# Performance work log

Hardware: AMD Instinct MI355X
Metric: run time of the kernel (lower is better)

## Reference

```python
import jax, jax.numpy as jnp
import numpy as np

B, E, P, L, D = 16, 2048, 16384, 5, 64  # batch, num_edges, num node-pairs, max_path_distance, edge_dim
EPS = 1e-9


def setup_inputs() -> dict:
    key = jax.random.key(0)
    k1, k2, k3 = jax.random.split(key, 3)
    edge_embedding = jax.random.normal(k1, (B, E, D), dtype=jnp.float32)
    # -1 marks padding (unused path slots), valid entries in [0, E)
    edge_paths = jax.random.randint(k2, (B, P, L), -1, E, dtype=jnp.int64)
    edge_vector = jax.random.normal(k3, (L, D), dtype=jnp.float32)
    return {"edge_embedding": edge_embedding, "edge_paths": edge_paths, "edge_vector": edge_vector}


def reference(edge_embedding, edge_paths, edge_vector):
    # edge_embedding: (B, E, D); edge_paths: (B, P, L) int with -1 padding; edge_vector: (L, D)
    edge_mask = edge_paths == -1                                     # (B, P, L)
    clamped = jnp.clip(edge_paths, 0, None)
    # batched gather: out[b, p, l, :] = edge_embedding[b, clamped[b, p, l], :]
    gathered = jax.vmap(lambda emb, idx: emb[idx])(edge_embedding, clamped)  # (B, P, L, D)
    gathered = jnp.where(edge_mask[..., None], jnp.zeros((), gathered.dtype), gathered)
    path_lengths = (~edge_mask).sum(axis=-1).astype(edge_embedding.dtype) + EPS  # (B, P)
    enc = jnp.einsum('beld,ld->be', gathered, edge_vector)           # (B, P)
    return enc / path_lengths
```

## Files before the change

### kernel.cpp

```cpp
#include <hip/hip_runtime.h>
#include <hip/hip_bf16.h>

#define B 16
#define E 2048
#define P 16384
#define L 5
#define D 64
#define EPS 1e-9f

__global__ __launch_bounds__(256) void edge_proj_kernel(
    const float* __restrict__ emb, const float* __restrict__ ev,
    float* __restrict__ proj) {
    __shared__ float sev[L * D];
    for (int i = threadIdx.x; i < L * D; i += 256) sev[i] = ev[i];
    __syncthreads();

    int gid  = blockIdx.x * 256 + threadIdx.x;
    int row  = gid >> 1;
    int half = gid & 1;

    const float4* src = (const float4*)(emb + (size_t)row * D + half * 32);
    const float4* w4  = (const float4*)sev;

    float acc[L] = {0.f, 0.f, 0.f, 0.f, 0.f};
#pragma unroll
    for (int c = 0; c < 8; ++c) {
        float4 v = src[c];
#pragma unroll
        for (int l = 0; l < L; ++l) {
            float4 w = w4[l * 16 + half * 8 + c];
            acc[l] += v.x * w.x + v.y * w.y + v.z * w.z + v.w * w.w;
        }
    }
#pragma unroll
    for (int l = 0; l < L; ++l) acc[l] += __shfl_xor(acc[l], 1);

    if (half == 0) {
        float* p = proj + (size_t)row * L;
#pragma unroll
        for (int l = 0; l < L; ++l) p[l] = acc[l];
    }
}

__global__ __launch_bounds__(256) void edge_gather_kernel(
    const int* __restrict__ paths, const float* __restrict__ proj,
    float* __restrict__ out) {
    __shared__ float sproj[E * L];
    int b = blockIdx.x & 15;
    int g = blockIdx.x >> 4;

    const float4* src = (const float4*)(proj + (size_t)b * E * L);
    float4* dst = (float4*)sproj;
#pragma unroll
    for (int i = 0; i < (E * L) / 4 / 256; ++i)
        dst[threadIdx.x + i * 256] = src[threadIdx.x + i * 256];
    __syncthreads();

    int pbase = g * (P / 16);
#pragma unroll
    for (int k = 0; k < 4; ++k) {
        int p = pbase + k * 256 + threadIdx.x;
        const int* pp = paths + ((size_t)b * P + p) * L;
        float sum = 0.f;
        int cnt = 0;
#pragma unroll
        for (int l = 0; l < L; ++l) {
            int e = pp[l];
            bool valid = (e >= 0);
            int ec = valid ? e : 0;
            float v = sproj[ec * L + l];
            sum += valid ? v : 0.f;
            cnt += valid ? 1 : 0;
        }
        out[(size_t)b * P + p] = sum / ((float)cnt + EPS);
    }
}

extern "C" void kernel_launch(void* const* d_in, const int* in_sizes, int n_in,
                              void* d_out, int out_size, void* d_ws, size_t ws_size,
                              hipStream_t stream) {
    const float* emb   = (const float*)d_in[0];
    const int*   paths = (const int*)d_in[1];
    const float* ev    = (const float*)d_in[2];
    float* out  = (float*)d_out;
    float* proj = (float*)d_ws;

    edge_proj_kernel<<<(2 * B * E) / 256, 256, 0, stream>>>(emb, ev, proj);
    edge_gather_kernel<<<16 * B, 256, 0, stream>>>(paths, proj, out);
}
```

Baseline: 68.47 us.

## Fuse edge projection into gather kernel with per-block recomputation

Merges the projection and gather kernels into one launch: each block recomputes the per-edge projections for its batch directly into shared memory, then performs the path gather. This removes a kernel launch and the global workspace round-trip for the projection. In exchange, each of the 16 blocks per batch redundantly reads the full batch embedding and redoes the projection, with many accumulators per thread and strided row reads.

```diff
diff --git a/kernel.cpp b/kernel.cpp
--- a/kernel.cpp
+++ b/kernel.cpp
@@ -8,59 +8,62 @@
 #define D 64
 #define EPS 1e-9f
 
-__global__ __launch_bounds__(256) void edge_proj_kernel(
-    const float* __restrict__ emb, const float* __restrict__ ev,
-    float* __restrict__ proj) {
+__global__ __launch_bounds__(256) void edge_fused_kernel(
+    const float* __restrict__ emb, const int* __restrict__ paths,
+    const float* __restrict__ ev, float* __restrict__ out) {
+    __shared__ float sproj[E * L];
     __shared__ float sev[L * D];
-    for (int i = threadIdx.x; i < L * D; i += 256) sev[i] = ev[i];
+
+    const int t = threadIdx.x;
+    const int b = blockIdx.x & 15;
+    const int g = blockIdx.x >> 4;
+
+    for (int i = t; i < L * D; i += 256) sev[i] = ev[i];
     __syncthreads();
 
-    int gid  = blockIdx.x * 256 + threadIdx.x;
-    int row  = gid >> 1;
-    int half = gid & 1;
+    {
+        const float4* __restrict__ rb =
+            (const float4*)(emb + ((size_t)b * E + t) * D);
+        const float4* __restrict__ w4 = (const float4*)sev;
 
-    const float4* src = (const float4*)(emb + (size_t)row * D + half * 32);
-    const float4* w4  = (const float4*)sev;
+        float accx[8][L], accy[8][L];
+#pragma unroll
+        for (int r = 0; r < 8; ++r)
+#pragma unroll
+            for (int l = 0; l < L; ++l) { accx[r][l] = 0.f; accy[r][l] = 0.f; }
 
-    float acc[L] = {0.f, 0.f, 0.f, 0.f, 0.f};
 #pragma unroll
-    for (int c = 0; c < 8; ++c) {
-        float4 v = src[c];
+        for (int c = 0; c < D / 4; ++c) {
+            float4 w[L];
 #pragma unroll
-        for (int l = 0; l < L; ++l) {
-            float4 w = w4[l * 16 + half * 8 + c];
-            acc[l] += v.x * w.x + v.y * w.y + v.z * w.z + v.w * w.w;
+            for (int l = 0; l < L; ++l) w[l] = w4[l * (D / 4) + c];
+#pragma unroll
+            for (int r = 0; r < 8; ++r) {
+                float4 v = rb[r * (256 * D / 4) + c];
+#pragma unroll
+                for (int l = 0; l < L; ++l) {
+                    accx[r][l] = fmaf(v.x, w[l].x, accx[r][l]);
+                    accy[r][l] = fmaf(v.y, w[l].y, accy[r][l]);
+                    accx[r][l] = fmaf(v.z, w[l].z, accx[r][l]);
+                    accy[r][l] = fmaf(v.w, w[l].w, accy[r][l]);
+                }
+            }
+        }
+#pragma unroll
+        for (int r = 0; r < 8; ++r) {
+            int e = t + r * 256;
+#pragma unroll
+            for (int l = 0; l < L; ++l)
+                sproj[e * L + l] = accx[r][l] + accy[r][l];
         }
     }
-#pragma unroll
-    for (int l = 0; l < L; ++l) acc[l] += __shfl_xor(acc[l], 1);
-
-    if (half == 0) {
-        float* p = proj + (size_t)row * L;
-#pragma unroll
-        for (int l = 0; l < L; ++l) p[l] = acc[l];
-    }
-}
-
-__global__ __launch_bounds__(256) void edge_gather_kernel(
-    const int* __restrict__ paths, const float* __restrict__ proj,
-    float* __restrict__ out) {
-    __shared__ float sproj[E * L];
-    int b = blockIdx.x & 15;
-    int g = blockIdx.x >> 4;
-
-    const float4* src = (const float4*)(proj + (size_t)b * E * L);
-    float4* dst = (float4*)sproj;
-#pragma unroll
-    for (int i = 0; i < (E * L) / 4 / 256; ++i)
-        dst[threadIdx.x + i * 256] = src[threadIdx.x + i * 256];
     __syncthreads();
 
-    int pbase = g * (P / 16);
+    const int pbase = g * (P / 16);
 #pragma unroll
     for (int k = 0; k < 4; ++k) {
-        int p = pbase + k * 256 + threadIdx.x;
-        const int* pp = paths + ((size_t)b * P + p) * L;
+        int p = pbase + k * 256 + t;
+        const int* __restrict__ pp = paths + ((size_t)b * P + p) * L;
         float sum = 0.f;
         int cnt = 0;
 #pragma unroll
@@ -82,9 +85,7 @@
     const float* emb   = (const float*)d_in[0];
     const int*   paths = (const int*)d_in[1];
     const float* ev    = (const float*)d_in[2];
-    float* out  = (float*)d_out;
-    float* proj = (float*)d_ws;
+    float* out = (float*)d_out;
 
-    edge_proj_kernel<<<(2 * B * E) / 256, 256, 0, stream>>>(emb, ev, proj);
-    edge_gather_kernel<<<16 * B, 256, 0, stream>>>(paths, proj, out);
+    edge_fused_kernel<<<16 * B, 256, 0, stream>>>(emb, paths, ev, out);
 }
```

Result: slower. 94.44 us (+37.9%).
